# Performance work log

Hardware: AMD Instinct MI355X
Metric: run time of the kernel (lower is better)

## Reference

```python
import jax, jax.numpy as jnp
import numpy as np

B, L, D, C, N, K = 4096, 4096, 1024, 64, 8192, 5
TEMP = 0.1
ALPHA = 2.0
EPS = 1e-12


def setup_inputs() -> dict:
    key = jax.random.key(0)
    ks = jax.random.split(key, 8)
    x = jax.random.normal(ks[0], (B, 1, L), jnp.float32)
    y = jax.random.randint(ks[1], (B,), 0, C)
    Wf = jax.random.normal(ks[2], (L, D), jnp.float32) * 0.02
    Wc = jax.random.normal(ks[3], (C, D), jnp.float32) * 0.02
    bc = jnp.zeros((C,), jnp.float32)
    supports_old = jax.random.normal(ks[4], (N, D), jnp.float32)
    scores_old = jax.nn.softmax(jax.random.normal(ks[5], (N, C), jnp.float32), axis=-1)
    labels_old = jax.nn.one_hot(jax.random.randint(ks[6], (N,), 0, C), C, dtype=jnp.float32)
    return dict(x=x, y=y, Wf=Wf, Wc=Wc, bc=bc, supports_old=supports_old,
                labels_old=labels_old, scores_old=scores_old)


def _l2n(v, axis):
    return v / jnp.maximum(jnp.linalg.norm(v, axis=axis, keepdims=True), EPS)


def _masked_mean(v, w):
    return jnp.sum(v * w) / jnp.maximum(jnp.sum(w), 1.0)


def _tta_loss(x, Wf, Wc, bc, supports_old, labels_old, scores_old):
    feats = x.reshape(B, L) @ Wf                      # [B, D] featurizer
    logits = feats @ Wc.T + bc                        # [B, C]
    probs = jax.nn.softmax(logits, -1)
    logp = jax.nn.log_softmax(logits, -1)
    prob = probs.max(-1)
    pred = jnp.argmax(logits, -1)
    # prediction-confidence filter
    y_certain = prob >= prob.mean()
    # input-energy entropy filter (scipy.stats.entropy over axis=2)
    px = x * x
    px = px / jnp.maximum(px.sum(2, keepdims=True), EPS)
    e = -(px * jnp.log(px + 1e-30)).sum(2).reshape(B)
    e_certain = e < e.mean()
    w_c = (e_certain & y_certain).astype(jnp.float32)  # certain mask as weights
    w_u = 1.0 - w_c
    yhat = jax.nn.one_hot(pred, C, dtype=jnp.float32)
    # --- memory bank concat + prototype build (no_grad in torch) ---
    sup_all = jnp.concatenate([supports_old, feats], 0)        # [N+B, D]
    lab_all = jnp.concatenate([labels_old, yhat], 0)           # [N+B, C]
    w_all = jnp.concatenate([jnp.ones((N,), jnp.float32), w_c], 0)
    lw = lab_all * w_all[:, None]
    protos = _l2n(sup_all, 1).T @ lw / jnp.maximum(lw.sum(0, keepdims=True), EPS)
    protos = jax.lax.stop_gradient(_l2n(protos, 0))            # [D, C]
    # --- loss1: Tsallis entropy - diversity on balanced probs ---
    m = jnp.sum(probs * w_c[:, None], 0) / jnp.maximum(w_c.sum(), 1.0)
    pb = probs / jnp.maximum(m, EPS)
    pb = pb / pb.sum(1, keepdims=True)
    tsallis = jnp.mean((1.0 - jnp.sum(pb ** ALPHA, 1)) / (ALPHA - 1.0))
    pm = pb.mean(0)
    div = -jnp.sum(pm * jnp.log(pm + EPS))
    loss1 = tsallis - div
    # --- loss2: PCL, prototype CE on certain samples (temp=1) ---
    lp = jax.nn.log_softmax(_l2n(feats, 1) @ protos, -1)       # [B, C]
    ce = -jnp.take_along_axis(lp, pred[:, None], 1)[:, 0]
    loss2 = _masked_mean(ce, w_c)
    # --- loss3: NCL, kNN soft targets from memory bank, uncertain rows ---
    scores_all = jax.lax.stop_gradient(jnp.concatenate([scores_old, probs], 0))
    sup_det = jax.lax.stop_gradient(sup_all)
    sim = _l2n(feats, 1) @ _l2n(sup_det, 1).T / TEMP           # [B, N+B]
    sim = jnp.where(w_all[None, :] > 0, sim, -jnp.inf)
    _, idx = jax.lax.top_k(sim, K)                             # [B, K]
    tgt = scores_all[idx].mean(1)                              # [B, C]
    ncl = -(tgt * logp).sum(1)
    loss3 = _masked_mean(ncl, w_u)
    return loss1 + loss2 + loss3


def reference(x, y, Wf, Wc, bc, supports_old, labels_old, scores_old):
    return _tta_loss(x, Wf, Wc, bc, supports_old, labels_old, scores_old)
```

## Files before the change

### kernel.cpp

```cpp
#include <hip/hip_runtime.h>
#include <math.h>

#define BBATCH 4096
#define LLEN   4096
#define DDIM   1024
#define CCLS   64
#define NSUP   8192
#define NTOT   12288
#define FEPS   1e-12f
#define KCHUNK 96
#define KCAND  (KCHUNK*5)

#define SC_SUMP  0
#define SC_SUME  1
#define SC_SUMWC 2
#define SC_TSAL  3
#define SC_L2NUM 4
#define SC_L3NUM 5

typedef _Float16 half4_t __attribute__((ext_vector_type(4)));
typedef _Float16 half8_t __attribute__((ext_vector_type(8)));
typedef float    f32x4   __attribute__((ext_vector_type(4)));
typedef float    f32x16  __attribute__((ext_vector_type(16)));

static const size_t OFF_FEATS  = 0;
static const size_t OFF_FEATP1 = OFF_FEATS  + (size_t)BBATCH*DDIM;
static const size_t OFF_WFTH   = OFF_FEATP1 + (size_t)BBATCH*DDIM;
static const size_t OFF_WFTL   = OFF_WFTH   + (size_t)DDIM*LLEN/2;
static const size_t OFF_PROBS  = OFF_WFTL   + (size_t)DDIM*LLEN/2;
static const size_t OFF_LOGP   = OFF_PROBS  + (size_t)BBATCH*CCLS;
static const size_t OFF_FNORM  = OFF_LOGP   + (size_t)BBATCH*CCLS;
static const size_t OFF_SNORM  = OFF_FNORM  + BBATCH;
static const size_t OFF_PMAX   = OFF_SNORM  + NSUP;
static const size_t OFF_EROW   = OFF_PMAX   + BBATCH;
static const size_t OFF_WC     = OFF_EROW   + BBATCH;
static const size_t OFF_PRED   = OFF_WC     + BBATCH;
static const size_t OFF_RB     = OFF_PRED   + BBATCH;
static const size_t OFF_SNM    = OFF_RB     + BBATCH;
static const size_t OFF_PROTOT = OFF_SNM    + NTOT;
static const size_t OFF_CVAL   = OFF_PROTOT + (size_t)CCLS*DDIM;
static const size_t OFF_CIDX   = OFF_CVAL   + (size_t)BBATCH*KCAND;
static const size_t OFF_ZERO   = OFF_CIDX   + (size_t)BBATCH*KCAND;
static const size_t OFF_MACC   = OFF_ZERO;
static const size_t OFF_PMACC  = OFF_MACC   + CCLS;
static const size_t OFF_COLS   = OFF_PMACC  + CCLS;
static const size_t OFF_SCAL   = OFF_COLS   + CCLS;
static const size_t OFF_PROTUN = OFF_SCAL   + 32;
static const size_t OFF_ZEND   = OFF_PROTUN + (size_t)DDIM*CCLS;
static const size_t OFF_SUPH   = OFF_ZEND;
static const size_t OFF_SUPL   = OFF_SUPH   + (size_t)NSUP*DDIM/2;
static const size_t WS_END     = OFF_SUPL   + (size_t)NSUP*DDIM/2;

__device__ __forceinline__ float waveSum(float v){
  #pragma unroll
  for (int o = 32; o > 0; o >>= 1) v += __shfl_xor(v, o);
  return v;
}
__device__ __forceinline__ float waveMax(float v){
  #pragma unroll
  for (int o = 32; o > 0; o >>= 1) v = fmaxf(v, __shfl_xor(v, o));
  return v;
}
__device__ __forceinline__ float blockSum256(float v, float* sh4){
  v = waveSum(v);
  if ((threadIdx.x & 63) == 0) sh4[threadIdx.x >> 6] = v;
  __syncthreads();
  float r = sh4[0] + sh4[1] + sh4[2] + sh4[3];
  __syncthreads();
  return r;
}
__device__ __forceinline__ void top5_insert(float* v, int* ix, float s, int si){
  bool c0 = s > v[0], c1 = s > v[1], c2 = s > v[2], c3 = s > v[3], c4 = s > v[4];
  v[4] = c4 ? (c3 ? v[3] : s) : v[4];  ix[4] = c4 ? (c3 ? ix[3] : si) : ix[4];
  v[3] = c3 ? (c2 ? v[2] : s) : v[3];  ix[3] = c3 ? (c2 ? ix[2] : si) : ix[3];
  v[2] = c2 ? (c1 ? v[1] : s) : v[2];  ix[2] = c2 ? (c1 ? ix[1] : si) : ix[2];
  v[1] = c1 ? (c0 ? v[0] : s) : v[1];  ix[1] = c1 ? (c0 ? ix[0] : si) : ix[1];
  v[0] = c0 ? s : v[0];                ix[0] = c0 ? si : ix[0];
}
__device__ __forceinline__ void split4(const float4 v, half4_t* h, half4_t* l){
  half4_t hh, ll;
  hh[0] = (_Float16)v.x; hh[1] = (_Float16)v.y; hh[2] = (_Float16)v.z; hh[3] = (_Float16)v.w;
  ll[0] = (_Float16)(v.x - (float)hh[0]);
  ll[1] = (_Float16)(v.y - (float)hh[1]);
  ll[2] = (_Float16)(v.z - (float)hh[2]);
  ll[3] = (_Float16)(v.w - (float)hh[3]);
  *h = hh; *l = ll;
}
__device__ __forceinline__ void split8(const float4 a, const float4 b,
                                       half8_t* h, half8_t* l){
  half8_t hh, ll;
  hh[0]=(_Float16)a.x; hh[1]=(_Float16)a.y; hh[2]=(_Float16)a.z; hh[3]=(_Float16)a.w;
  hh[4]=(_Float16)b.x; hh[5]=(_Float16)b.y; hh[6]=(_Float16)b.z; hh[7]=(_Float16)b.w;
  ll[0]=(_Float16)(a.x-(float)hh[0]); ll[1]=(_Float16)(a.y-(float)hh[1]);
  ll[2]=(_Float16)(a.z-(float)hh[2]); ll[3]=(_Float16)(a.w-(float)hh[3]);
  ll[4]=(_Float16)(b.x-(float)hh[4]); ll[5]=(_Float16)(b.y-(float)hh[5]);
  ll[6]=(_Float16)(b.z-(float)hh[6]); ll[7]=(_Float16)(b.w-(float)hh[7]);
  *h = hh; *l = ll;
}

__global__ __launch_bounds__(256)
void k_entropy(const float* __restrict__ x, float* __restrict__ e_row,
               float* __restrict__ scal){
  __shared__ __align__(16) float lx[LLEN];
  __shared__ float sh4[4];
  int row = blockIdx.x, t = threadIdx.x;
  const float4* xr = (const float4*)(x + (size_t)row * LLEN);
  float s = 0.f;
  #pragma unroll
  for (int i = 0; i < 4; ++i){
    float4 v = xr[t + 256*i];
    ((float4*)lx)[t + 256*i] = v;
    s += v.x*v.x + v.y*v.y + v.z*v.z + v.w*v.w;
  }
  s = blockSum256(s, sh4);
  float inv = 1.0f / fmaxf(s, FEPS);
  float ent = 0.f;
  #pragma unroll
  for (int i = 0; i < 4; ++i){
    float4 v = ((float4*)lx)[t + 256*i];
    float p;
    p = v.x*v.x*inv; ent -= p * logf(p + 1e-30f);
    p = v.y*v.y*inv; ent -= p * logf(p + 1e-30f);
    p = v.z*v.z*inv; ent -= p * logf(p + 1e-30f);
    p = v.w*v.w*inv; ent -= p * logf(p + 1e-30f);
  }
  ent = blockSum256(ent, sh4);
  if (t == 0){ e_row[row] = ent; atomicAdd(&scal[SC_SUME], ent); }
}

__global__ __launch_bounds__(256)
void k_wft(const float* __restrict__ Wf, unsigned short* __restrict__ WftH,
           unsigned short* __restrict__ WftL){
  __shared__ __align__(16) float ld[64*68];
  int t = threadIdx.x;
  int d0 = blockIdx.x * 64;
  int l0 = blockIdx.y * 64;
  #pragma unroll
  for (int i = 0; i < 4; ++i){
    int flat = t + 256*i;
    int l = flat >> 4, d4 = (flat & 15) * 4;
    *(float4*)&ld[l*68 + d4] = *(const float4*)(Wf + (size_t)(l0+l)*DDIM + d0 + d4);
  }
  __syncthreads();
  #pragma unroll
  for (int i = 0; i < 4; ++i){
    int flat = t + 256*i;
    int d = flat >> 4, l4 = (flat & 15) * 4;
    float4 v = make_float4(ld[(l4+0)*68 + d], ld[(l4+1)*68 + d],
                           ld[(l4+2)*68 + d], ld[(l4+3)*68 + d]);
    half4_t h, l;
    split4(v, &h, &l);
    *(half4_t*)(WftH + (size_t)(d0+d)*LLEN + l0 + l4) = h;
    *(half4_t*)(WftL + (size_t)(d0+d)*LLEN + l0 + l4) = l;
  }
}

#define SUBH 4096

__global__ __launch_bounds__(256)
void k_feats_mfma(const float* __restrict__ X, const unsigned short* __restrict__ WftHu,
                  const unsigned short* __restrict__ WftLu, float* __restrict__ featp){
  __shared__ __align__(16) _Float16 lds[2*4*SUBH];
  int t = threadIdx.x;
  int n0 = blockIdx.x * 128;
  int m0 = blockIdx.y * 128;
  int kz = blockIdx.z;
  int w = t >> 6, lane = t & 63;
  int wr = w >> 1, wc = w & 1;
  int l31 = lane & 31, hi = lane >> 5;
  const _Float16* Bgh = (const _Float16*)WftHu + (size_t)n0*LLEN;
  const _Float16* Bgl = (const _Float16*)WftLu + (size_t)n0*LLEN;
  const size_t glRow = (size_t)(lane >> 2)*LLEN;
  int ra = t >> 1;
  int kg8 = (t & 1) * 16;
  int aswz = (ra >> 3) & 3;
  const float* Ag = X + (size_t)(m0 + ra)*LLEN + kg8;
  f32x16 acc[2][2];
  #pragma unroll
  for (int i=0;i<2;++i){
    #pragma unroll
    for (int j=0;j<2;++j) acc[i][j] = (f32x16)(0.f);
  }
  const int kstart = kz*2048;

  #define STAGE_B(bufi, k0c) do {                                                 \
    _Float16* Lb = lds + (bufi)*(4*SUBH);                                         \
    _Pragma("unroll")                                                             \
    for (int s2 = 0; s2 < 2; ++s2){                                               \
      int blk = s2*4 + w;                                                         \
      int csrc = (lane & 3) ^ ((blk*2 + (lane >> 5)) & 3);                        \
      size_t go = glRow + (size_t)blk*16*LLEN + (k0c) + (size_t)csrc*8;           \
      __builtin_amdgcn_global_load_lds(                                           \
        (const __attribute__((address_space(1))) void*)(Bgh + go),                \
        (__attribute__((address_space(3))) void*)(Lb + 2*SUBH + blk*512), 16,0,0);\
      __builtin_amdgcn_global_load_lds(                                           \
        (const __attribute__((address_space(1))) void*)(Bgl + go),                \
        (__attribute__((address_space(3))) void*)(Lb + 3*SUBH + blk*512), 16,0,0);\
    }                                                                             \
  } while(0)

  STAGE_B(0, kstart);
  float4 avs[4];
  #pragma unroll
  for (int i=0;i<4;++i) avs[i] = *(const float4*)(Ag + kstart + 4*i);
  int cur = 0;
  int swz = (l31 >> 3) & 3;
  for (int it = 0; it < 64; ++it){
    _Float16* Ah = lds + cur*(4*SUBH);
    _Float16* Al = Ah + SUBH;
    #pragma unroll
    for (int c2 = 0; c2 < 2; ++c2){
      half8_t hv, lv;
      split8(avs[2*c2], avs[2*c2+1], &hv, &lv);
      int slot = ((kg8 >> 3) + c2) ^ aswz;
      *(half8_t*)&Ah[ra*32 + slot*8] = hv;
      *(half8_t*)&Al[ra*32 + slot*8] = lv;
    }
    __syncthreads();
    if (it < 63){
      int kn = kstart + (it+1)*32;
      STAGE_B(cur ^ 1, kn);
      #pragma unroll
      for (int i=0;i<4;++i) avs[i] = *(const float4*)(Ag + kn + 4*i);
      __builtin_amdgcn_sched_barrier(0);
    }
    const _Float16* Bh = lds + cur*(4*SUBH) + 2*SUBH;
    const _Float16* Bl = Bh + SUBH;
    #pragma unroll
    for (int kf = 0; kf < 2; ++kf){
      int sc = (kf*2 + hi) ^ swz;
      half8_t ahf[2], alf[2], bhf[2], blf[2];
      #pragma unroll
      for (int mi=0;mi<2;++mi){
        int off = (wr*64 + mi*32 + l31)*32 + sc*8;
        ahf[mi] = *(const half8_t*)&Ah[off];
        alf[mi] = *(const half8_t*)&Al[off];
      }
      #pragma unroll
      for (int ni=0;ni<2;++ni){
        int off = (wc*64 + ni*32 + l31)*32 + sc*8;
        bhf[ni] = *(const half8_t*)&Bh[off];
        blf[ni] = *(const half8_t*)&Bl[off];
      }
      #pragma unroll
      for (int mi=0;mi<2;++mi){
        #pragma unroll
        for (int ni=0;ni<2;++ni){
          acc[mi][ni] = __builtin_amdgcn_mfma_f32_32x32x16_f16(ahf[mi], bhf[ni], acc[mi][ni], 0,0,0);
          acc[mi][ni] = __builtin_amdgcn_mfma_f32_32x32x16_f16(ahf[mi], blf[ni], acc[mi][ni], 0,0,0);
          acc[mi][ni] = __builtin_amdgcn_mfma_f32_32x32x16_f16(alf[mi], bhf[ni], acc[mi][ni], 0,0,0);
        }
      }
    }
    cur ^= 1;
  }
  #undef STAGE_B
  float* outp = featp + (size_t)kz * BBATCH * DDIM;
  #pragma unroll
  for (int mi=0;mi<2;++mi){
    #pragma unroll
    for (int ni=0;ni<2;++ni){
      #pragma unroll
      for (int r=0;r<16;++r){
        int row = m0 + wr*64 + mi*32 + (r&3) + 8*(r>>2) + 4*hi;
        int col = n0 + wc*64 + ni*32 + l31;
        outp[(size_t)row*DDIM + col] = acc[mi][ni][r];
      }
    }
  }
}

__global__ __launch_bounds__(256)
void k_supnorm(const float* __restrict__ sup, float* __restrict__ snorm,
               _Float16* __restrict__ suph, _Float16* __restrict__ supl){
  int w = threadIdx.x >> 6, lane = threadIdx.x & 63;
  int row = blockIdx.x*4 + w;
  const float4* rp = (const float4*)(sup + (size_t)row * DDIM);
  float s = 0.f;
  #pragma unroll
  for (int j=0;j<4;++j){
    float4 v = rp[lane + 64*j];
    half4_t h, l;
    split4(v, &h, &l);
    *(half4_t*)(suph + (size_t)row*DDIM + (lane + 64*j)*4) = h;
    *(half4_t*)(supl + (size_t)row*DDIM + (lane + 64*j)*4) = l;
    s += v.x*v.x+v.y*v.y+v.z*v.z+v.w*v.w;
  }
  s = waveSum(s);
  if (lane==0) snorm[row] = sqrtf(s);
}

__global__ __launch_bounds__(256)
void k_logits(float* __restrict__ feats, const float* __restrict__ featp1,
              const float* __restrict__ Wc,
              const float* __restrict__ bc, float* __restrict__ probs,
              float* __restrict__ logp, float* __restrict__ pmax,
              int* __restrict__ pred, float* __restrict__ fnorm,
              float* __restrict__ scal,
              _Float16* __restrict__ fh, _Float16* __restrict__ fl){
  __shared__ __align__(16) float f[DDIM];
  __shared__ float z[CCLS];
  __shared__ float sh4[4];
  int row = blockIdx.x, t = threadIdx.x;
  const float4* fr0 = (const float4*)(feats  + (size_t)row * DDIM);
  const float4* fr1 = (const float4*)(featp1 + (size_t)row * DDIM);
  float ss = 0.f;
  { float4 a = fr0[t], b = fr1[t];
    float4 v = make_float4(a.x+b.x, a.y+b.y, a.z+b.z, a.w+b.w);
    ((float4*)f)[t] = v;
    ((float4*)(feats + (size_t)row*DDIM))[t] = v;
    half4_t h, l;
    split4(v, &h, &l);
    *(half4_t*)(fh + (size_t)row*DDIM + t*4) = h;
    *(half4_t*)(fl + (size_t)row*DDIM + t*4) = l;
    ss += v.x*v.x+v.y*v.y+v.z*v.z+v.w*v.w; }
  ss = blockSum256(ss, sh4);
  if (t==0) fnorm[row] = sqrtf(ss);
  int w = t >> 6, lane = t & 63;
  for (int ci = 0; ci < 16; ++ci){
    int c = w*16 + ci;
    const float4* wc = (const float4*)(Wc + (size_t)c * DDIM);
    float d = 0.f;
    #pragma unroll
    for (int j=0;j<4;++j){
      float4 a = wc[lane + 64*j];
      float4 b = ((float4*)f)[lane + 64*j];
      d += a.x*b.x+a.y*b.y+a.z*b.z+a.w*b.w;
    }
    d = waveSum(d);
    if (lane == 0) z[c] = d + bc[c];
  }
  __syncthreads();
  if (w == 0){
    float zz = z[lane];
    float m = waveMax(zz);
    unsigned long long bal = __ballot(zz == m);
    int am = __ffsll(bal) - 1;
    float ex = expf(zz - m);
    float sv = waveSum(ex);
    probs[(size_t)row*CCLS + lane] = ex / sv;
    logp[(size_t)row*CCLS + lane]  = (zz - m) - logf(sv);
    if (lane == 0){
      float pmv = 1.0f / sv;
      pmax[row] = pmv;
      pred[row] = am;
      atomicAdd(&scal[SC_SUMP], pmv);
    }
  }
}

__global__ __launch_bounds__(256)
void k_mask(const float* __restrict__ e_row, const float* __restrict__ pmax,
            const float* __restrict__ fnorm, const float* __restrict__ snorm,
            const int* __restrict__ pred, float* __restrict__ w_c,
            float* __restrict__ rb, float* __restrict__ snm,
            float* __restrict__ colsum, float* __restrict__ scal){
  int i = blockIdx.x * 256 + threadIdx.x;
  if (i < NSUP) snm[i] = 1.0f / fmaxf(snorm[i], FEPS);
  if (i < BBATCH){
    float me = scal[SC_SUME] * (1.0f/BBATCH);
    float mp = scal[SC_SUMP] * (1.0f/BBATCH);
    float wc = ((e_row[i] < me) && (pmax[i] >= mp)) ? 1.0f : 0.0f;
    w_c[i] = wc;
    float fn = fmaxf(fnorm[i], FEPS);
    rb[i] = 10.0f / fn;
    snm[NSUP + i] = (wc > 0.f) ? (1.0f / fn) : -1.0f;
    atomicAdd(&scal[SC_SUMWC], wc);
    atomicAdd(&colsum[pred[i]], wc);
  }
}

__global__ __launch_bounds__(256)
void k_colsum_labels(const float* __restrict__ labels, float* __restrict__ colsum){
  int t = threadIdx.x, c = t & 63, sub = t >> 6;
  int r0 = blockIdx.x * 256;
  float s = 0.f;
  for (int i = 0; i < 64; ++i){
    int r = r0 + sub + 4*i;
    s += labels[(size_t)r*CCLS + c];
  }
  __shared__ float loc[4][64];
  loc[sub][c] = s;
  __syncthreads();
  if (sub == 0) atomicAdd(&colsum[c], loc[0][c]+loc[1][c]+loc[2][c]+loc[3][c]);
}

__global__ __launch_bounds__(256)
void k_m_accum(const float* __restrict__ probs, const float* __restrict__ w_c,
               float* __restrict__ m_acc){
  int t = threadIdx.x, c = t & 63, sub = t >> 6;
  int r0 = blockIdx.x * 64;
  float s = 0.f;
  for (int i = 0; i < 16; ++i){
    int r = r0 + sub + 4*i;
    s += probs[(size_t)r*CCLS + c] * w_c[r];
  }
  __shared__ float loc[4][64];
  loc[sub][c] = s;
  __syncthreads();
  if (sub == 0) atomicAdd(&m_acc[c], loc[0][c]+loc[1][c]+loc[2][c]+loc[3][c]);
}

__global__ __launch_bounds__(256)
void k_loss1(const float* __restrict__ probs, const float* __restrict__ m_acc,
             float* __restrict__ pm_acc, float* __restrict__ scal){
  int t = threadIdx.x, w = t >> 6, lane = t & 63;
  float swc = fmaxf(scal[SC_SUMWC], 1.0f);
  float minv = 1.0f / fmaxf(m_acc[lane] / swc, FEPS);
  float pml = 0.f, tsl = 0.f;
  int r0 = blockIdx.x * 64 + w * 16;
  for (int i = 0; i < 16; ++i){
    int r = r0 + i;
    float pb = probs[(size_t)r*CCLS + lane] * minv;
    float t1 = waveSum(pb);
    float t2 = waveSum(pb*pb);
    tsl += 1.0f - t2/(t1*t1);
    pml += pb/t1;
  }
  atomicAdd(&pm_acc[lane], pml);
  if (lane == 0) atomicAdd(&scal[SC_TSAL], tsl);
}

__global__ __launch_bounds__(256)
void k_protos_gemm(const float* __restrict__ sup, const float* __restrict__ feats,
                   const float* __restrict__ labels, const int* __restrict__ pred,
                   const float* __restrict__ w_c, const float* __restrict__ snm,
                   float* __restrict__ protos_un){
  __shared__ __align__(16) float ssx[64*68];
  __shared__ __align__(16) float sl[64*68];
  int t = threadIdx.x;
  int d0 = blockIdx.x * 64;
  int nbase = blockIdx.y * 1536;
  int dg = t & 15, cg = t >> 4;
  float acc[4][4];
  #pragma unroll
  for (int i=0;i<4;++i){
    #pragma unroll
    for (int j=0;j<4;++j) acc[i][j]=0.f;
  }
  for (int n0 = 0; n0 < 1536; n0 += 64){
    __syncthreads();
    #pragma unroll
    for (int i = 0; i < 4; ++i){
      int fidx = t + 256*i;
      int r = fidx >> 4;
      int dc = (fidx & 15) * 4;
      int n = nbase + n0 + r;
      const float* rp = (n < NSUP) ? (sup + (size_t)n*DDIM)
                                   : (feats + (size_t)(n-NSUP)*DDIM);
      *(float4*)&ssx[r*68 + dc] = *(const float4*)(rp + d0 + dc);
    }
    #pragma unroll
    for (int i = 0; i < 4; ++i){
      int fidx = t + 256*i;
      int r = fidx >> 4;
      int cc = (fidx & 15) * 4;
      int n = nbase + n0 + r;
      float sc = snm[n];
      float4 v;
      if (n < NSUP){
        float4 lb = *(const float4*)(labels + (size_t)n*CCLS + cc);
        v.x = lb.x*sc; v.y = lb.y*sc; v.z = lb.z*sc; v.w = lb.w*sc;
      } else {
        int b = n - NSUP;
        float base = w_c[b] * sc;
        int p = pred[b];
        v.x = (p == cc+0) ? base : 0.f;
        v.y = (p == cc+1) ? base : 0.f;
        v.z = (p == cc+2) ? base : 0.f;
        v.w = (p == cc+3) ? base : 0.f;
      }
      *(float4*)&sl[r*68 + cc] = v;
    }
    __syncthreads();
    #pragma unroll 4
    for (int kk = 0; kk < 64; ++kk){
      float4 a = *(float4*)&ssx[kk*68 + 4*dg];
      float4 b = *(float4*)&sl[kk*68 + 4*cg];
      float av[4] = {a.x,a.y,a.z,a.w};
      float bv[4] = {b.x,b.y,b.z,b.w};
      #pragma unroll
      for (int i=0;i<4;++i){
        #pragma unroll
        for (int j=0;j<4;++j) acc[i][j] = fmaf(av[i], bv[j], acc[i][j]);
      }
    }
  }
  #pragma unroll
  for (int i=0;i<4;++i){
    #pragma unroll
    for (int j=0;j<4;++j)
      atomicAdd(&protos_un[(size_t)(d0 + 4*dg + i)*CCLS + 4*cg + j], acc[i][j]);
  }
}

__global__ __launch_bounds__(256)
void k_protos_norm(const float* __restrict__ protos_un, const float* __restrict__ colsum,
                   float* __restrict__ protos_t){
  int c = blockIdx.x, t = threadIdx.x;
  __shared__ float sh4[4];
  float cs = fmaxf(colsum[c], FEPS);
  float v[4];
  float ss = 0.f;
  #pragma unroll
  for (int i=0;i<4;++i){
    int d = t + 256*i;
    v[i] = protos_un[(size_t)d*CCLS + c] / cs;
    ss += v[i]*v[i];
  }
  ss = blockSum256(ss, sh4);
  float inv = 1.0f / fmaxf(sqrtf(ss), FEPS);
  #pragma unroll
  for (int i=0;i<4;++i){
    int d = t + 256*i;
    protos_t[(size_t)c*DDIM + d] = v[i]*inv;
  }
}

__global__ __launch_bounds__(256)
void k_loss2(const float* __restrict__ feats, const float* __restrict__ protos_t,
             const int* __restrict__ pred, const float* __restrict__ w_c,
             const float* __restrict__ fnorm, float* __restrict__ scal){
  int row = blockIdx.x, t = threadIdx.x;
  float wc = w_c[row];
  if (wc == 0.f) return;
  __shared__ __align__(16) float f[DDIM];
  __shared__ float z[CCLS];
  float inv = 1.0f / fmaxf(fnorm[row], FEPS);
  { float4 v = ((const float4*)(feats + (size_t)row*DDIM))[t];
    v.x*=inv; v.y*=inv; v.z*=inv; v.w*=inv;
    ((float4*)f)[t] = v; }
  __syncthreads();
  int w = t >> 6, lane = t & 63;
  for (int ci=0; ci<16; ++ci){
    int c = w*16+ci;
    const float4* pc = (const float4*)(protos_t + (size_t)c*DDIM);
    float d = 0.f;
    #pragma unroll
    for (int j=0;j<4;++j){
      float4 a = pc[lane + 64*j];
      float4 b = ((float4*)f)[lane + 64*j];
      d += a.x*b.x+a.y*b.y+a.z*b.z+a.w*b.w;
    }
    d = waveSum(d);
    if (lane==0) z[c] = d;
  }
  __syncthreads();
  if (w == 0){
    float zz = z[lane];
    float m = waveMax(zz);
    float sv = waveSum(expf(zz - m));
    if (lane == 0){
      float lse = m + logf(sv);
      float ce = lse - z[pred[row]];
      atomicAdd(&scal[SC_L2NUM], ce * wc);
    }
  }
}

__global__ __launch_bounds__(256)
void k_sim_mfma(const _Float16* __restrict__ fh, const _Float16* __restrict__ fl,
                const _Float16* __restrict__ suph, const _Float16* __restrict__ supl,
                const float* __restrict__ rb, const float* __restrict__ snm,
                float* __restrict__ cval, int* __restrict__ cidx){
  __shared__ __align__(16) _Float16 lds[2*4*SUBH];
  __shared__ float sns[128];
  int t = threadIdx.x;
  int m0 = blockIdx.x * 128;
  int n0 = blockIdx.y * 128;
  int w = t >> 6, lane = t & 63;
  int wr = w >> 1, wc = w & 1;
  int l31 = lane & 31, hi = lane >> 5;
  if (t < 128) sns[t] = snm[m0 + t];
  const _Float16* Agh; const _Float16* Agl;
  if (blockIdx.x < 64){ Agh = suph + (size_t)m0*DDIM; Agl = supl + (size_t)m0*DDIM; }
  else                { Agh = fh + (size_t)(m0-NSUP)*DDIM; Agl = fl + (size_t)(m0-NSUP)*DDIM; }
  const _Float16* Bgh = fh + (size_t)n0*DDIM;
  const _Float16* Bgl = fl + (size_t)n0*DDIM;
  const size_t glRow = (size_t)(lane >> 2) * DDIM;
  f32x16 acc[2][2];
  #pragma unroll
  for (int i=0;i<2;++i){
    #pragma unroll
    for (int j=0;j<2;++j) acc[i][j] = (f32x16)(0.f);
  }

  #define STAGE(bufi, k0c) do {                                                  \
    _Float16* Lb = lds + (bufi)*(4*SUBH);                                        \
    _Pragma("unroll")                                                            \
    for (int s2 = 0; s2 < 2; ++s2){                                              \
      int blk = s2*4 + w;                                                        \
      int csrc = (lane & 3) ^ ((blk*2 + (lane >> 5)) & 3);                       \
      size_t go = glRow + (size_t)blk*16*DDIM + (k0c) + (size_t)csrc*8;          \
      __builtin_amdgcn_global_load_lds(                                          \
        (const __attribute__((address_space(1))) void*)(Agh + go),               \
        (__attribute__((address_space(3))) void*)(Lb + 0*SUBH + blk*512), 16,0,0);\
      __builtin_amdgcn_global_load_lds(                                          \
        (const __attribute__((address_space(1))) void*)(Agl + go),               \
        (__attribute__((address_space(3))) void*)(Lb + 1*SUBH + blk*512), 16,0,0);\
      __builtin_amdgcn_global_load_lds(                                          \
        (const __attribute__((address_space(1))) void*)(Bgh + go),               \
        (__attribute__((address_space(3))) void*)(Lb + 2*SUBH + blk*512), 16,0,0);\
      __builtin_amdgcn_global_load_lds(                                          \
        (const __attribute__((address_space(1))) void*)(Bgl + go),               \
        (__attribute__((address_space(3))) void*)(Lb + 3*SUBH + blk*512), 16,0,0);\
    }                                                                            \
  } while(0)

  STAGE(0, 0);
  __syncthreads();
  int cur = 0;
  int swz = (l31 >> 3) & 3;
  for (int it = 0; it < 32; ++it){
    if (it < 31) STAGE(cur ^ 1, (it + 1) * 32);
    const _Float16* Ah = lds + cur*(4*SUBH);
    const _Float16* Al = Ah + SUBH;
    const _Float16* Bh = Ah + 2*SUBH;
    const _Float16* Bl = Ah + 3*SUBH;
    #pragma unroll
    for (int kf = 0; kf < 2; ++kf){
      int sc = (kf*2 + hi) ^ swz;
      half8_t ahf[2], alf[2], bhf[2], blf[2];
      #pragma unroll
      for (int mi=0;mi<2;++mi){
        int off = (wr*64 + mi*32 + l31)*32 + sc*8;
        ahf[mi] = *(const half8_t*)&Ah[off];
        alf[mi] = *(const half8_t*)&Al[off];
      }
      #pragma unroll
      for (int ni=0;ni<2;++ni){
        int off = (wc*64 + ni*32 + l31)*32 + sc*8;
        bhf[ni] = *(const half8_t*)&Bh[off];
        blf[ni] = *(const half8_t*)&Bl[off];
      }
      #pragma unroll
      for (int mi=0;mi<2;++mi){
        #pragma unroll
        for (int ni=0;ni<2;++ni){
          acc[mi][ni] = __builtin_amdgcn_mfma_f32_32x32x16_f16(ahf[mi], bhf[ni], acc[mi][ni], 0,0,0);
          acc[mi][ni] = __builtin_amdgcn_mfma_f32_32x32x16_f16(ahf[mi], blf[ni], acc[mi][ni], 0,0,0);
          acc[mi][ni] = __builtin_amdgcn_mfma_f32_32x32x16_f16(alf[mi], bhf[ni], acc[mi][ni], 0,0,0);
        }
      }
    }
    __syncthreads();
    cur ^= 1;
  }
  #undef STAGE
  float tv[2][5]; int ti[2][5];
  #pragma unroll
  for (int ni=0;ni<2;++ni){
    #pragma unroll
    for (int k=0;k<5;++k){ tv[ni][k] = -INFINITY; ti[ni][k] = 0x7fffffff; }
  }
  #pragma unroll
  for (int ni=0;ni<2;++ni){
    float rbv = rb[n0 + wc*64 + ni*32 + l31];
    #pragma unroll
    for (int mi=0;mi<2;++mi){
      #pragma unroll
      for (int r=0;r<16;++r){
        int rl = wr*64 + mi*32 + (r&3) + 8*(r>>2) + 4*hi;
        float sn = sns[rl];
        float v = acc[mi][ni][r] * rbv * fabsf(sn);
        v = (sn > 0.f) ? v : -INFINITY;
        top5_insert(tv[ni], ti[ni], v, m0 + rl);
      }
    }
  }
  #pragma unroll
  for (int ni=0;ni<2;++ni){
    float pv[5]; int pi[5];
    #pragma unroll
    for (int k=0;k<5;++k){ pv[k] = __shfl_xor(tv[ni][k], 32); pi[k] = __shfl_xor(ti[ni][k], 32); }
    #pragma unroll
    for (int k=0;k<5;++k) top5_insert(tv[ni], ti[ni], pv[k], pi[k]);
  }
  __syncthreads();
  float* MV = (float*)lds;
  int*   MI = (int*)(lds + 8192);
  if (hi == 0){
    #pragma unroll
    for (int ni=0;ni<2;++ni){
      int col = wc*64 + ni*32 + l31;
      #pragma unroll
      for (int k=0;k<5;++k){
        MV[(col*2 + wr)*5 + k] = tv[ni][k];
        MI[(col*2 + wr)*5 + k] = ti[ni][k];
      }
    }
  }
  __syncthreads();
  if (t < 128){
    float bv[5]; int bi[5];
    #pragma unroll
    for (int k=0;k<5;++k){ bv[k] = MV[(t*2+0)*5 + k]; bi[k] = MI[(t*2+0)*5 + k]; }
    #pragma unroll
    for (int k=0;k<5;++k) top5_insert(bv, bi, MV[(t*2+1)*5 + k], MI[(t*2+1)*5 + k]);
    float* co = cval + (size_t)(n0 + t)*KCAND + blockIdx.x*5;
    int*   ci = cidx + (size_t)(n0 + t)*KCAND + blockIdx.x*5;
    #pragma unroll
    for (int k=0;k<5;++k){ co[k] = bv[k]; ci[k] = bi[k]; }
  }
}

__global__ __launch_bounds__(256)
void k_merge_ncl(const float* __restrict__ cval, const int* __restrict__ cidx,
                 const float* __restrict__ scores_old, const float* __restrict__ probs,
                 const float* __restrict__ logp, const float* __restrict__ w_c,
                 float* __restrict__ scal){
  int t = threadIdx.x, w = t >> 6, lane = t & 63;
  int b = blockIdx.x*4 + w;
  float bv[5]; int bi[5];
  #pragma unroll
  for (int k=0;k<5;++k){ bv[k] = -INFINITY; bi[k] = 0x7fffffff; }
  #pragma unroll
  for (int it = 0; it < 8; ++it){
    int j = lane + 64*it;
    if (j < KCAND)
      top5_insert(bv, bi, cval[(size_t)b*KCAND + j], cidx[(size_t)b*KCAND + j]);
  }
  #pragma unroll
  for (int off = 32; off > 0; off >>= 1){
    float pv[5]; int pi[5];
    #pragma unroll
    for (int k=0;k<5;++k){ pv[k] = __shfl_xor(bv[k], off); pi[k] = __shfl_xor(bi[k], off); }
    #pragma unroll
    for (int k=0;k<5;++k) top5_insert(bv, bi, pv[k], pi[k]);
  }
  float tg = 0.f;
  #pragma unroll
  for (int k=0;k<5;++k){
    int ix = bi[k];
    const float* srow = (ix < NSUP) ? (scores_old + (size_t)ix*CCLS)
                                    : (probs + (size_t)(ix-NSUP)*CCLS);
    tg += srow[lane];
  }
  tg *= 0.2f;
  float d = tg * logp[(size_t)b*CCLS + lane];
  d = waveSum(d);
  if (lane == 0) atomicAdd(&scal[SC_L3NUM], -d * (1.0f - w_c[b]));
}

__global__ void k_final(const float* __restrict__ pm_acc, const float* __restrict__ scal,
                        float* __restrict__ out){
  int lane = threadIdx.x;
  float pm = pm_acc[lane] * (1.0f/BBATCH);
  float dterm = pm * logf(pm + FEPS);
  float dv = waveSum(dterm);
  if (lane == 0){
    float div = -dv;
    float tsallis = scal[SC_TSAL] * (1.0f/BBATCH);
    float swc = scal[SC_SUMWC];
    float l1 = tsallis - div;
    float l2 = scal[SC_L2NUM] / fmaxf(swc, 1.0f);
    float l3 = scal[SC_L3NUM] / fmaxf((float)BBATCH - swc, 1.0f);
    out[0] = l1 + l2 + l3;
  }
}

extern "C" void kernel_launch(void* const* d_in, const int* in_sizes, int n_in,
                              void* d_out, int out_size, void* d_ws, size_t ws_size,
                              hipStream_t stream){
  (void)in_sizes; (void)n_in; (void)out_size; (void)ws_size;
  const float* x      = (const float*)d_in[0];
  const float* Wf     = (const float*)d_in[2];
  const float* Wc     = (const float*)d_in[3];
  const float* bc     = (const float*)d_in[4];
  const float* sup    = (const float*)d_in[5];
  const float* labels = (const float*)d_in[6];
  const float* scores = (const float*)d_in[7];
  float* ws = (float*)d_ws;

  float* feats  = ws + OFF_FEATS;
  float* featp1 = ws + OFF_FEATP1;
  unsigned short* wfth = (unsigned short*)(ws + OFF_WFTH);
  unsigned short* wftl = (unsigned short*)(ws + OFF_WFTL);
  _Float16* feat_h = (_Float16*)(ws + OFF_WFTH);
  _Float16* feat_l = (_Float16*)(ws + OFF_WFTL);
  _Float16* sup_h  = (_Float16*)(ws + OFF_SUPH);
  _Float16* sup_l  = (_Float16*)(ws + OFF_SUPL);
  float* probs  = ws + OFF_PROBS;
  float* logp   = ws + OFF_LOGP;
  float* fnorm  = ws + OFF_FNORM;
  float* snorm  = ws + OFF_SNORM;
  float* pmax   = ws + OFF_PMAX;
  float* e_row  = ws + OFF_EROW;
  float* w_c    = ws + OFF_WC;
  int*   pred   = (int*)(ws + OFF_PRED);
  float* rb     = ws + OFF_RB;
  float* snm    = ws + OFF_SNM;
  float* protot = ws + OFF_PROTOT;
  float* cvalp  = ws + OFF_CVAL;
  int*   cidxp  = (int*)(ws + OFF_CIDX);
  float* m_acc  = ws + OFF_MACC;
  float* pm_acc = ws + OFF_PMACC;
  float* colsum = ws + OFF_COLS;
  float* scal   = ws + OFF_SCAL;
  float* protun = ws + OFF_PROTUN;

  hipMemsetAsync(ws + OFF_ZERO, 0, (OFF_ZEND - OFF_ZERO)*sizeof(float), stream);

  k_entropy      <<<BBATCH, 256, 0, stream>>>(x, e_row, scal);
  k_wft          <<<dim3(DDIM/64, LLEN/64), 256, 0, stream>>>(Wf, wfth, wftl);
  k_feats_mfma   <<<dim3(DDIM/128, BBATCH/128, 2), 256, 0, stream>>>(x, wfth, wftl, feats);
  k_supnorm      <<<NSUP/4, 256, 0, stream>>>(sup, snorm, sup_h, sup_l);
  k_logits       <<<BBATCH, 256, 0, stream>>>(feats, featp1, Wc, bc, probs, logp, pmax, pred, fnorm, scal, feat_h, feat_l);
  k_mask         <<<32, 256, 0, stream>>>(e_row, pmax, fnorm, snorm, pred, w_c, rb, snm, colsum, scal);
  k_colsum_labels<<<32, 256, 0, stream>>>(labels, colsum);
  k_m_accum      <<<64, 256, 0, stream>>>(probs, w_c, m_acc);
  k_loss1        <<<64, 256, 0, stream>>>(probs, m_acc, pm_acc, scal);
  k_protos_gemm  <<<dim3(16, 8), 256, 0, stream>>>(sup, feats, labels, pred, w_c, snm, protun);
  k_protos_norm  <<<CCLS, 256, 0, stream>>>(protun, colsum, protot);
  k_loss2        <<<BBATCH, 256, 0, stream>>>(feats, protot, pred, w_c, fnorm, scal);
  k_sim_mfma     <<<dim3(KCHUNK, BBATCH/128), 256, 0, stream>>>(feat_h, feat_l, sup_h, sup_l, rb, snm, cvalp, cidxp);
  k_merge_ncl    <<<BBATCH/4, 256, 0, stream>>>(cvalp, cidxp, scores, probs, logp, w_c, scal);
  k_final        <<<1, 64, 0, stream>>>(pm_acc, scal, (float*)d_out);
}
```

Baseline: 923.5 us.

## Enlarge similarity GEMM tiles to 256x256 with 512 threads and XCD-aware block mapping

The kNN similarity MFMA kernel moves from 128x128 tiles with 256 threads to 256x256 tiles with 512 threads (8 waves, each computing 128x64). This doubles operand reuse per LDS load and halves the candidate count per row that the merge kernel must scan. Block IDs are remapped so that blocks sharing the same feature columns land on the same XCD for L2 locality. Global-to-LDS prefetch is interleaved with the MFMA phases, using setprio and sched barriers. The cost is higher register and LDS pressure per block and fewer blocks in the grid (768 instead of 3072).

Measured after the change: 921.9 us. Within noise of the previous version (-0.2%).

```diff
diff --git a/kernel.cpp b/kernel.cpp
--- a/kernel.cpp
+++ b/kernel.cpp
@@ -8,7 +8,7 @@
 #define NSUP   8192
 #define NTOT   12288
 #define FEPS   1e-12f
-#define KCHUNK 96
+#define KCHUNK 48
 #define KCAND  (KCHUNK*5)
 
 #define SC_SUMP  0
@@ -558,95 +558,106 @@
   }
 }
 
-__global__ __launch_bounds__(256)
+#define SIMTILES 32
+__global__ __launch_bounds__(512, 2)
 void k_sim_mfma(const _Float16* __restrict__ fh, const _Float16* __restrict__ fl,
                 const _Float16* __restrict__ suph, const _Float16* __restrict__ supl,
                 const float* __restrict__ rb, const float* __restrict__ snm,
                 float* __restrict__ cval, int* __restrict__ cidx){
-  __shared__ __align__(16) _Float16 lds[2*4*SUBH];
-  __shared__ float sns[128];
+  __shared__ __align__(16) _Float16 lds[2*32768];
+  __shared__ float sns[256];
   int t = threadIdx.x;
-  int m0 = blockIdx.x * 128;
-  int n0 = blockIdx.y * 128;
   int w = t >> 6, lane = t & 63;
-  int wr = w >> 1, wc = w & 1;
+  int wr = w >> 2, wcn = w & 3;
   int l31 = lane & 31, hi = lane >> 5;
-  if (t < 128) sns[t] = snm[m0 + t];
-  const _Float16* Agh; const _Float16* Agl;
-  if (blockIdx.x < 64){ Agh = suph + (size_t)m0*DDIM; Agl = supl + (size_t)m0*DDIM; }
-  else                { Agh = fh + (size_t)(m0-NSUP)*DDIM; Agl = fl + (size_t)(m0-NSUP)*DDIM; }
+  int bidl = blockIdx.y * 48 + blockIdx.x;
+  int xcd = bidl & 7, lin = bidl >> 3;
+  int yb = xcd * 2 + (lin / 48);
+  int xb = lin - (lin / 48) * 48;
+  int m0 = xb * 256, n0 = yb * 256;
+  if (t < 256) sns[t] = snm[m0 + t];
+  const _Float16 *Agh, *Agl;
+  if (xb < 32){ Agh = suph + (size_t)m0*DDIM; Agl = supl + (size_t)m0*DDIM; }
+  else        { Agh = fh + (size_t)(m0-NSUP)*DDIM; Agl = fl + (size_t)(m0-NSUP)*DDIM; }
   const _Float16* Bgh = fh + (size_t)n0*DDIM;
   const _Float16* Bgl = fl + (size_t)n0*DDIM;
-  const size_t glRow = (size_t)(lane >> 2) * DDIM;
-  f32x16 acc[2][2];
-  #pragma unroll
-  for (int i=0;i<2;++i){
+  int Rlo = w*16 + (lane>>2), Rhi = 128 + Rlo;
+  size_t offLo = (size_t)Rlo*DDIM + (size_t)((((lane&3) ^ ((Rlo>>3)&3))) * 8);
+  size_t offHi = (size_t)Rhi*DDIM + (size_t)((((lane&3) ^ ((Rhi>>3)&3))) * 8);
+  const _Float16* srcArr[4] = {Agh, Agl, Bgh, Bgl};
+  f32x16 acc[4][2];
+  #pragma unroll
+  for (int i=0;i<4;++i){
     #pragma unroll
     for (int j=0;j<2;++j) acc[i][j] = (f32x16)(0.f);
   }
 
-  #define STAGE(bufi, k0c) do {                                                  \
-    _Float16* Lb = lds + (bufi)*(4*SUBH);                                        \
-    _Pragma("unroll")                                                            \
-    for (int s2 = 0; s2 < 2; ++s2){                                              \
-      int blk = s2*4 + w;                                                        \
-      int csrc = (lane & 3) ^ ((blk*2 + (lane >> 5)) & 3);                       \
-      size_t go = glRow + (size_t)blk*16*DDIM + (k0c) + (size_t)csrc*8;          \
-      __builtin_amdgcn_global_load_lds(                                          \
-        (const __attribute__((address_space(1))) void*)(Agh + go),               \
-        (__attribute__((address_space(3))) void*)(Lb + 0*SUBH + blk*512), 16,0,0);\
-      __builtin_amdgcn_global_load_lds(                                          \
-        (const __attribute__((address_space(1))) void*)(Agl + go),               \
-        (__attribute__((address_space(3))) void*)(Lb + 1*SUBH + blk*512), 16,0,0);\
-      __builtin_amdgcn_global_load_lds(                                          \
-        (const __attribute__((address_space(1))) void*)(Bgh + go),               \
-        (__attribute__((address_space(3))) void*)(Lb + 2*SUBH + blk*512), 16,0,0);\
-      __builtin_amdgcn_global_load_lds(                                          \
-        (const __attribute__((address_space(1))) void*)(Bgl + go),               \
-        (__attribute__((address_space(3))) void*)(Lb + 3*SUBH + blk*512), 16,0,0);\
-    }                                                                            \
+  #define SIM_STAGE(b, c, kt) do {                                                \
+    const _Float16* sp = srcArr[(c)>>1] + (((c)&1) ? offHi : offLo)               \
+                         + (size_t)(kt)*32;                                       \
+    __builtin_amdgcn_global_load_lds(                                             \
+      (const __attribute__((address_space(1))) void*)sp,                          \
+      (__attribute__((address_space(3))) void*)(lds + (b)*32768 + ((c)>>1)*8192   \
+                                                + ((c)&1)*4096 + w*512), 16,0,0); \
   } while(0)
 
-  STAGE(0, 0);
-  __syncthreads();
-  int cur = 0;
-  int swz = (l31 >> 3) & 3;
-  for (int it = 0; it < 32; ++it){
-    if (it < 31) STAGE(cur ^ 1, (it + 1) * 32);
-    const _Float16* Ah = lds + cur*(4*SUBH);
-    const _Float16* Al = Ah + SUBH;
-    const _Float16* Bh = Ah + 2*SUBH;
-    const _Float16* Bl = Ah + 3*SUBH;
-    #pragma unroll
-    for (int kf = 0; kf < 2; ++kf){
-      int sc = (kf*2 + hi) ^ swz;
-      half8_t ahf[2], alf[2], bhf[2], blf[2];
-      #pragma unroll
-      for (int mi=0;mi<2;++mi){
-        int off = (wr*64 + mi*32 + l31)*32 + sc*8;
-        ahf[mi] = *(const half8_t*)&Ah[off];
-        alf[mi] = *(const half8_t*)&Al[off];
-      }
-      #pragma unroll
-      for (int ni=0;ni<2;++ni){
-        int off = (wc*64 + ni*32 + l31)*32 + sc*8;
-        bhf[ni] = *(const half8_t*)&Bh[off];
-        blf[ni] = *(const half8_t*)&Bl[off];
-      }
-      #pragma unroll
-      for (int mi=0;mi<2;++mi){
+  SIM_STAGE(0,0,0); SIM_STAGE(0,1,0); SIM_STAGE(0,2,0); SIM_STAGE(0,3,0);
+  SIM_STAGE(0,4,0); SIM_STAGE(0,5,0); SIM_STAGE(0,6,0); SIM_STAGE(0,7,0);
+
+  for (int kt = 0; kt < SIMTILES; ++kt){
+    const _Float16* buf = lds + (kt&1)*32768;
+    int nb = (kt+1)&1;
+    asm volatile("s_waitcnt vmcnt(0)" ::: "memory");
+    __builtin_amdgcn_s_barrier();
+    __builtin_amdgcn_sched_barrier(0);
+    half8_t bh[2][2], bl[2][2];
+    #pragma unroll
+    for (int ni=0;ni<2;++ni){
+      int Rb = wcn*64 + ni*32 + l31;
+      int swB = (Rb>>3)&3;
+      const _Float16* pbh = buf + 16384 + Rb*32;
+      const _Float16* pbl = buf + 24576 + Rb*32;
+      #pragma unroll
+      for (int k=0;k<2;++k){
+        int s = ((k*2+hi)^swB)*8;
+        bh[ni][k] = *(const half8_t*)(pbh + s);
+        bl[ni][k] = *(const half8_t*)(pbl + s);
+      }
+    }
+    #pragma unroll
+    for (int p=0;p<4;++p){
+      int Ra = wr*128 + p*32 + l31;
+      int swA = (Ra>>3)&3;
+      const _Float16* pah = buf + Ra*32;
+      const _Float16* pal = buf + 8192 + Ra*32;
+      half8_t ah[2], al[2];
+      #pragma unroll
+      for (int k=0;k<2;++k){
+        int s = ((k*2+hi)^swA)*8;
+        ah[k] = *(const half8_t*)(pah + s);
+        al[k] = *(const half8_t*)(pal + s);
+      }
+      if (kt < SIMTILES-1){
+        if (p==0){ SIM_STAGE(nb,0,kt+1); SIM_STAGE(nb,1,kt+1); }
+        else if (p==1){ SIM_STAGE(nb,2,kt+1); SIM_STAGE(nb,3,kt+1); SIM_STAGE(nb,4,kt+1); }
+        else if (p==2){ SIM_STAGE(nb,5,kt+1); SIM_STAGE(nb,6,kt+1); SIM_STAGE(nb,7,kt+1); }
+      }
+      __builtin_amdgcn_s_setprio(1);
+      #pragma unroll
+      for (int k=0;k<2;++k){
         #pragma unroll
         for (int ni=0;ni<2;++ni){
-          acc[mi][ni] = __builtin_amdgcn_mfma_f32_32x32x16_f16(ahf[mi], bhf[ni], acc[mi][ni], 0,0,0);
-          acc[mi][ni] = __builtin_amdgcn_mfma_f32_32x32x16_f16(ahf[mi], blf[ni], acc[mi][ni], 0,0,0);
-          acc[mi][ni] = __builtin_amdgcn_mfma_f32_32x32x16_f16(alf[mi], bhf[ni], acc[mi][ni], 0,0,0);
+          acc[p][ni] = __builtin_amdgcn_mfma_f32_32x32x16_f16(ah[k], bh[ni][k], acc[p][ni], 0,0,0);
+          acc[p][ni] = __builtin_amdgcn_mfma_f32_32x32x16_f16(ah[k], bl[ni][k], acc[p][ni], 0,0,0);
+          acc[p][ni] = __builtin_amdgcn_mfma_f32_32x32x16_f16(al[k], bh[ni][k], acc[p][ni], 0,0,0);
         }
       }
-    }
-    __syncthreads();
-    cur ^= 1;
-  }
-  #undef STAGE
+      __builtin_amdgcn_s_setprio(0);
+      __builtin_amdgcn_sched_barrier(0);
+    }
+  }
+  #undef SIM_STAGE
+  __syncthreads();
   float tv[2][5]; int ti[2][5];
   #pragma unroll
   for (int ni=0;ni<2;++ni){
@@ -655,12 +666,12 @@
   }
   #pragma unroll
   for (int ni=0;ni<2;++ni){
-    float rbv = rb[n0 + wc*64 + ni*32 + l31];
-    #pragma unroll
-    for (int mi=0;mi<2;++mi){
+    float rbv = rb[n0 + wcn*64 + ni*32 + l31];
+    #pragma unroll
+    for (int mi=0;mi<4;++mi){
       #pragma unroll
       for (int r=0;r<16;++r){
-        int rl = wr*64 + mi*32 + (r&3) + 8*(r>>2) + 4*hi;
+        int rl = wr*128 + mi*32 + (r&3) + 8*(r>>2) + 4*hi;
         float sn = sns[rl];
         float v = acc[mi][ni][r] * rbv * fabsf(sn);
         v = (sn > 0.f) ? v : -INFINITY;
@@ -676,13 +687,12 @@
     #pragma unroll
     for (int k=0;k<5;++k) top5_insert(tv[ni], ti[ni], pv[k], pi[k]);
   }
-  __syncthreads();
   float* MV = (float*)lds;
-  int*   MI = (int*)(lds + 8192);
+  int*   MI = (int*)(lds + 5120);
   if (hi == 0){
     #pragma unroll
     for (int ni=0;ni<2;++ni){
-      int col = wc*64 + ni*32 + l31;
+      int col = wcn*64 + ni*32 + l31;
       #pragma unroll
       for (int k=0;k<5;++k){
         MV[(col*2 + wr)*5 + k] = tv[ni][k];
@@ -691,14 +701,14 @@
     }
   }
   __syncthreads();
-  if (t < 128){
+  if (t < 256){
     float bv[5]; int bi[5];
     #pragma unroll
     for (int k=0;k<5;++k){ bv[k] = MV[(t*2+0)*5 + k]; bi[k] = MI[(t*2+0)*5 + k]; }
     #pragma unroll
     for (int k=0;k<5;++k) top5_insert(bv, bi, MV[(t*2+1)*5 + k], MI[(t*2+1)*5 + k]);
-    float* co = cval + (size_t)(n0 + t)*KCAND + blockIdx.x*5;
-    int*   ci = cidx + (size_t)(n0 + t)*KCAND + blockIdx.x*5;
+    float* co = cval + (size_t)(n0 + t)*KCAND + xb*5;
+    int*   ci = cidx + (size_t)(n0 + t)*KCAND + xb*5;
     #pragma unroll
     for (int k=0;k<5;++k){ co[k] = bv[k]; ci[k] = bi[k]; }
   }
@@ -715,7 +725,7 @@
   #pragma unroll
   for (int k=0;k<5;++k){ bv[k] = -INFINITY; bi[k] = 0x7fffffff; }
   #pragma unroll
-  for (int it = 0; it < 8; ++it){
+  for (int it = 0; it < 4; ++it){
     int j = lane + 64*it;
     if (j < KCAND)
       top5_insert(bv, bi, cval[(size_t)b*KCAND + j], cidx[(size_t)b*KCAND + j]);
@@ -813,7 +823,7 @@
   k_protos_gemm  <<<dim3(16, 8), 256, 0, stream>>>(sup, feats, labels, pred, w_c, snm, protun);
   k_protos_norm  <<<CCLS, 256, 0, stream>>>(protun, colsum, protot);
   k_loss2        <<<BBATCH, 256, 0, stream>>>(feats, protot, pred, w_c, fnorm, scal);
-  k_sim_mfma     <<<dim3(KCHUNK, BBATCH/128), 256, 0, stream>>>(feat_h, feat_l, sup_h, sup_l, rb, snm, cvalp, cidxp);
+  k_sim_mfma     <<<dim3(48, 16), 512, 0, stream>>>(feat_h, feat_l, sup_h, sup_l, rb, snm, cvalp, cidxp);
   k_merge_ncl    <<<BBATCH/4, 256, 0, stream>>>(cvalp, cidxp, scores, probs, logp, w_c, scal);
   k_final        <<<1, 64, 0, stream>>>(pm_acc, scal, (float*)d_out);
 }
```
